# Kernel tuning notes

Hardware: AMD Instinct MI355X
Metric: run time of the kernel (lower is better)

The kernel has to match this reference:

```python
import jax, jax.numpy as jnp
import numpy as np

CANVAS = 512
SCORE_THR = 0.02
NMS_THR = 0.45
LVTOP = 1000      # cfg['lvtop'] for mm source
IMTOP = 200       # cfg['imtop']
NMS_PRE = 2000    # fixed pre-NMS candidate cap (static shape for jit)
NUM_CLASSES = 80
STRIDES = [8, 16, 32, 64, 128, 256, 512]
AR3 = [False, True, True, True, True, False, False]


def _make_priors():
    # get_scales(512): smallest=0.04, rmin=0.1, rmax=0.9, n=7
    smallest, rmin, rmax, n = 0.04, 0.1, 0.9, 7
    step = (rmax - rmin) / (n - 2)
    scales = [smallest] + [rmin + i * step for i in range(n)]
    sz = np.round(np.array(scales) * CANVAS).astype(np.int64)
    pr, lvlen = [], []
    for i, s in enumerate(STRIDES):
        fs = CANVAS // s
        ratios = [1.0, 2.0, 0.5] + ([3.0, 1.0 / 3.0] if AR3[i] else [])
        wh = [(sz[i] * np.sqrt(r), sz[i] / np.sqrt(r)) for r in ratios]
        extra = np.sqrt(float(sz[i]) * float(sz[i + 1]))  # sqrt(sz[i+1]/sz[i])*sz[i]
        wh.insert(1, (extra, extra))
        wh = np.array(wh, np.float32)            # [na, 2]
        xs = (np.arange(fs, dtype=np.float32) + 0.5) * s
        cx, cy = np.meshgrid(xs, xs)             # rows index y
        ctr = np.stack([cx, cy], -1)[:, :, None, :]  # [fs, fs, 1, 2]
        na = wh.shape[0]
        p = np.concatenate([np.broadcast_to(ctr, (fs, fs, na, 2)),
                            np.broadcast_to(wh, (fs, fs, na, 2))], -1).reshape(-1, 4)
        pr.append(p)
        lvlen.append(p.shape[0])
    return np.concatenate(pr).astype(np.float32), lvlen

PRIORS_NP, LVLEN = _make_priors()   # total 24564, lvlen=[16384,6144,1536,384,96,16,4]


def setup_inputs() -> dict:
    key = jax.random.key(0)
    k1, k2 = jax.random.split(key)
    A = PRIORS_NP.shape[0]
    cls_logits = jax.random.normal(k1, (4, A, NUM_CLASSES + 1), dtype=jnp.float32)
    reg = jax.random.normal(k2, (4, A, 4), dtype=jnp.float32)
    priors = jnp.asarray(PRIORS_NP)
    return {"cls_logits": cls_logits, "reg": reg, "priors": priors}


def _pairwise_iou(b):  # b: [K,4] xyxy
    area = (b[:, 2] - b[:, 0]) * (b[:, 3] - b[:, 1])
    lt = jnp.maximum(b[:, None, :2], b[None, :, :2])
    rb = jnp.minimum(b[:, None, 2:], b[None, :, 2:])
    wh = jnp.clip(rb - lt, 0.0)
    inter = wh[..., 0] * wh[..., 1]
    return inter / jnp.maximum(area[:, None] + area[None, :] - inter, 1e-6)


def _nms_keep(b):  # boxes sorted by descending score, class-offset applied
    m = _pairwise_iou(b) * jnp.triu(jnp.ones((NMS_PRE, NMS_PRE), b.dtype), 1)
    def body(sup, i):
        sup = sup | ((~sup[i]) & (m[i] > NMS_THR))
        return sup, None
    sup, _ = jax.lax.scan(body, jnp.zeros((NMS_PRE,), bool), jnp.arange(NMS_PRE))
    return ~sup


def reference(cls_logits, reg, priors):
    N = cls_logits.shape[0]
    C = NUM_CLASSES
    # softmax, background class is LAST (bckg_class_first=False for mm source)
    scr = jax.nn.softmax(cls_logits, axis=-1)[..., :-1]
    scr = jnp.where(scr > SCORE_THR, scr, 0.0)  # score threshold (fidx filter)
    # per-level top-k over flattened (anchor, class) pairs  [post.top_per_level]
    vals_l, anch_l, cls_l = [], [], []
    start = 0
    for lv in LVLEN:
        f = scr[:, start:start + lv, :].reshape(N, lv * C)
        k = min(LVTOP, lv * C)
        v, idx = jax.lax.top_k(f, k)
        vals_l.append(v)
        anch_l.append(start + idx // C)
        cls_l.append(idx % C)
        start += lv
    vals = jnp.concatenate(vals_l, 1)
    anch = jnp.concatenate(anch_l, 1)
    cls = jnp.concatenate(cls_l, 1)
    # fixed-size pre-NMS cap (static shapes under jit)
    v2, sel = jax.lax.top_k(vals, NMS_PRE)
    anch = jnp.take_along_axis(anch, sel, 1)
    cls = jnp.take_along_axis(cls, sel, 1)
    # decode boxes  [post.decode_boxes, mults=(0.1, 0.2), clamp=True]
    p = priors[anch]                                 # [N,K,4] cxcywh
    r = jnp.take_along_axis(reg, anch[..., None], 1)  # [N,K,4]
    cx = p[..., 0] + r[..., 0] * 0.1 * p[..., 2]
    cy = p[..., 1] + r[..., 1] * 0.1 * p[..., 3]
    w = p[..., 2] * jnp.exp(r[..., 2] * 0.2)
    h = p[..., 3] * jnp.exp(r[..., 3] * 0.2)
    boxes = jnp.stack([cx - w / 2, cy - h / 2, cx + w / 2, cy + h / 2], -1)
    boxes = jnp.clip(boxes, 0.0, float(CANVAS))
    # class-aware NMS via class offsets
    nb = boxes + cls.astype(boxes.dtype)[..., None] * (2.0 * CANVAS)
    keep = jax.vmap(_nms_keep)(nb)                   # [N,K] bool
    fs = jnp.where(keep & (v2 > 0), v2, 0.0)
    fv, fi = jax.lax.top_k(fs, IMTOP)                # imtop
    fb = jnp.take_along_axis(boxes, fi[..., None], 1)
    fc = jnp.take_along_axis(cls, fi, 1)
    fb = jnp.where(fv[..., None] > 0, fb, 0.0)
    return fb, fv, fc
```

## Files before the change

kernel.cpp:

```cpp
#include <hip/hip_runtime.h>
#include <hip/hip_bf16.h>
#include <math.h>

typedef unsigned long long u64;
typedef unsigned int u32;

#define A_TOTAL 24564
#define NCLS 80
#define NIMG 4
#define NPRE 2000
#define NLV 7
#define HBUCKETS 1024
#define BEXP_BASE 0x3CA3
#define TOTAL_G (NIMG * A_TOTAL)
#define FA 64
#define FT 256
#define NBLK_F ((TOTAL_G + FA - 1) / FA)
#define POOL_CAP_MAX 4096
#define CAPSEL 4608
#define MROWS 512
#define FTILES (MROWS / 16)

__device__ __constant__ int c_klv[NLV] = {1000,1000,1000,1000,1000,1000,320};

#define WS_HIST      0
#define WS_MCOUNT    114688
#define WS_BCOUNT    114800
#define WS_ZERO_END  114912
#define WS_PCOUNT    114912
#define WS_MAIN      121280
#define WS_BND       350656
#define WS_BOXES     1268160
#define WS_CLS       1396160
#define WS_SCORE     1428160
#define WS_MASK      1460160
#define WS_POOL      3508160

#define NZERO_W (WS_ZERO_END / 4)

__device__ inline u64 shfl_u64(u64 v, int src) {
  int lo = __shfl((int)(u32)(v & 0xFFFFFFFFULL), src);
  int hi = __shfl((int)(u32)(v >> 32), src);
  return ((u64)(u32)hi << 32) | (u32)lo;
}

__device__ inline int score_bucket(u32 bits) {
  int b = (int)(bits >> 16) - BEXP_BASE;
  return b < 0 ? 0 : (b > HBUCKETS - 1 ? HBUCKETS - 1 : b);
}

__device__ inline int level_of(int a) {
  return (a < 16384) ? 0 : (a < 22528) ? 1 : (a < 24064) ? 2 :
         (a < 24448) ? 3 : (a < 24544) ? 4 : (a < 24560) ? 5 : 6;
}

__global__ __launch_bounds__(256) void k_zero(u32* __restrict__ p) {
  int i = blockIdx.x * 256 + threadIdx.x;
  if (i < NZERO_W) p[i] = 0;
}

__device__ inline void score20(const float* __restrict__ logits, int g, int q,
                               float (&e)[20], float& rt) {
  const float* row = logits + (size_t)g * 81;
  float x[20];
#pragma unroll
  for (int i = 0; i < 20; ++i) x[i] = row[q + 4 * i];
  float x80 = (q == 3) ? row[80] : 0.f;
  float mloc = x[0];
#pragma unroll
  for (int i = 1; i < 20; ++i) mloc = fmaxf(mloc, x[i]);
  if (q == 3) mloc = fmaxf(mloc, x80);
  float m = fmaxf(mloc, __shfl_xor(mloc, 1));
  m = fmaxf(m, __shfl_xor(m, 2));
  float tq = 0.f;
#pragma unroll
  for (int i = 0; i < 20; ++i) { e[i] = expf(x[i] - m); tq += e[i]; }
  if (q == 3) tq += expf(x80 - m);
  float t = tq + __shfl_xor(tq, 1);
  t = t + __shfl_xor(t, 2);
  rt = 1.0f / t;
}

__device__ inline void wave_find_cut(const u32* __restrict__ h, int k, int lane,
                                     int& cx, int& cy) {
  u32 s = 0;
#pragma unroll
  for (int i = 0; i < 16; ++i) s += h[lane * 16 + i];
  u32 S = s;
#pragma unroll
  for (int o = 1; o < 64; o <<= 1) {
    u32 t = (u32)__shfl_down((int)S, o);
    if (lane + o < 64) S += t;
  }
  u32 total = (u32)__shfl((int)S, 0);
  if (total <= (u32)k) { cx = -1; cy = 0; return; }
  u64 bm = __ballot(S >= (u32)k);
  int L0 = 63 - (int)__clzll((long long)bm);
  u32 Sup = (u32)__shfl_down((int)S, 1);
  if (lane == 63) Sup = 0;
  int rcx = 0, rcy = 0;
  if (lane == L0) {
    u32 cum = Sup;
    for (int i = 15; i >= 0; --i) {
      u32 c = h[lane * 16 + i];
      if (cum + c >= (u32)k) { rcx = lane * 16 + i; rcy = k - (int)cum; break; }
      cum += c;
    }
  }
  cx = __shfl(rcx, L0);
  cy = __shfl(rcy, L0);
}

__global__ __launch_bounds__(FT) void k_fused(const float* __restrict__ logits,
                                              u32* __restrict__ histG,
                                              u64* __restrict__ pool,
                                              u32* __restrict__ pcount, int cap) {
  __shared__ u64 sh8_[HBUCKETS / 2];
  u32* sh = (u32*)sh8_;
  __shared__ int nm;
  int tid = threadIdx.x, bx = blockIdx.x;
  for (int b = tid; b < HBUCKETS; b += FT) sh[b] = 0;
  if (tid == 0) nm = 0;
  int la = tid >> 2, q = tid & 3;
  int g = bx * FA + la;
  bool valid = g < TOTAL_G;
  int g0 = bx * FA;
  int seg0 = (g0 / A_TOTAL) * NLV + level_of(g0 % A_TOTAL);
  int seg = seg0, a = 0;
  float e[20];
  float rt = 0.f;
  if (valid) {
    int img = g / A_TOTAL;
    a = g - img * A_TOTAL;
    seg = img * NLV + level_of(a);
    score20(logits, g, q, e, rt);
  }
  int uniform = __syncthreads_and((int)(!valid || seg == seg0));
  if (valid) {
    u32* hdst = uniform ? sh : (histG + (size_t)seg * HBUCKETS);
    u32 wmask = 0;
#pragma unroll
    for (int i = 0; i < 20; ++i) {
      float s = e[i] * rt;
      if (s > 0.02f) wmask |= (1u << i);
    }
    int cnt = __popc(wmask);
    int basep = 0;
    if (cnt) basep = atomicAdd(&nm, cnt);
    while (wmask) {
      int i = __ffs(wmask) - 1;
      wmask &= wmask - 1;
      float s = e[i] * rt;
      u32 bits = __float_as_uint(s);
      atomicAdd(&hdst[score_bucket(bits)], 1u);
      if (basep < cap)
        pool[(size_t)bx * cap + basep] =
            ((u64)bits << 32) | (u64)(0xFFFFFFFFu - (u32)(a * NCLS + q + 4 * i));
      ++basep;
    }
  }
  __syncthreads();
  if (uniform) {
    u64* hseg8 = (u64*)(histG + (size_t)seg0 * HBUCKETS);
    for (int b = tid; b < HBUCKETS / 2; b += FT) {
      u64 v = sh8_[b];
      if (v) atomicAdd(&hseg8[b], v);
    }
  }
  if (tid == 0) pcount[bx] = (u32)nm;
}

__global__ __launch_bounds__(FT) void k_filter(const float* __restrict__ logits,
                                               const u64* __restrict__ pool,
                                               const u32* __restrict__ pcount,
                                               const u32* __restrict__ histG, int cap,
                                               u64* __restrict__ mainG, u32* __restrict__ mcount,
                                               u64* __restrict__ bndG, u32* __restrict__ bcount) {
  __shared__ int lcx4[4];
  __shared__ u64 mk[1024]; __shared__ unsigned char msg_[1024];
  __shared__ u64 bkl[256]; __shared__ unsigned char bsg[256];
  __shared__ int nm, nb, cm[4], cb[4], basem[4], baseb[4], wm[4], wb[4];
  int tid = threadIdx.x, bx = blockIdx.x;
  if (tid < 4) { cm[tid] = 0; cb[tid] = 0; wm[tid] = 0; wb[tid] = 0; }
  if (tid == 0) { nm = 0; nb = 0; }
  int g0 = bx * FA;
  int img0 = g0 / A_TOTAL;
  int alo = g0 - img0 * A_TOTAL;
  int gN = g0 + FA - 1; if (gN > TOTAL_G - 1) gN = TOTAL_G - 1;
  int seg_lo = img0 * NLV + level_of(alo);
  int seg_hi = (gN / A_TOTAL) * NLV + level_of(gN % A_TOTAL);
  int nseg = seg_hi - seg_lo + 1;
  int wid = tid >> 6, lane = tid & 63;
  if (wid < nseg) {
    int cx, cy;
    wave_find_cut(histG + (size_t)(seg_lo + wid) * HBUCKETS,
                  c_klv[(seg_lo + wid) % NLV], lane, cx, cy);
    if (lane == 0) lcx4[wid] = cx;
  }
  __syncthreads();
  int n = (int)pcount[bx];
  if (n <= cap) {
    for (int t = tid; t < n; t += FT) {
      u64 key = pool[(size_t)bx * cap + t];
      u32 bits = (u32)(key >> 32);
      u32 flat = 0xFFFFFFFFu - (u32)(key & 0xFFFFFFFFULL);
      int a = (int)(flat / NCLS);
      int img = (a >= alo) ? img0 : img0 + 1;
      int seg = img * NLV + level_of(a);
      int si = seg - seg_lo;
      int ctx = lcx4[si];
      int bk = score_bucket(bits);
      if (ctx < 0 || bk > ctx) {
        int p = atomicAdd(&nm, 1);
        if (p < 1024) { mk[p] = key; msg_[p] = (unsigned char)si; atomicAdd(&cm[si], 1); }
        else { u32 pg = atomicAdd(&mcount[seg], 1u); if (pg < 1024) mainG[(size_t)seg * 1024 + pg] = key; }
      } else if (bk == ctx) {
        int p = atomicAdd(&nb, 1);
        if (p < 256) { bkl[p] = key; bsg[p] = (unsigned char)si; atomicAdd(&cb[si], 1); }
        else { u32 pg = atomicAdd(&bcount[seg], 1u); if (pg < 4096) bndG[(size_t)seg * 4096 + pg] = key; }
      }
    }
  } else {
    int la = tid >> 2, q = tid & 3;
    int g = g0 + la;
    if (g < TOTAL_G) {
      int img = g / A_TOTAL;
      int a = g - img * A_TOTAL;
      int seg = img * NLV + level_of(a);
      int si = seg - seg_lo;
      int ctx = lcx4[si];
      float e[20];
      float rt;
      score20(logits, g, q, e, rt);
      for (int i = 0; i < 20; ++i) {
        float s = e[i] * rt;
        if (s > 0.02f) {
          u32 bits = __float_as_uint(s);
          int bk = score_bucket(bits);
          u64 key = ((u64)bits << 32) | (u64)(0xFFFFFFFFu - (u32)(a * NCLS + q + 4 * i));
          if (ctx < 0 || bk > ctx) {
            int p = atomicAdd(&nm, 1);
            if (p < 1024) { mk[p] = key; msg_[p] = (unsigned char)si; atomicAdd(&cm[si], 1); }
            else { u32 pg = atomicAdd(&mcount[seg], 1u); if (pg < 1024) mainG[(size_t)seg * 1024 + pg] = key; }
          } else if (bk == ctx) {
            int p = atomicAdd(&nb, 1);
            if (p < 256) { bkl[p] = key; bsg[p] = (unsigned char)si; atomicAdd(&cb[si], 1); }
            else { u32 pg = atomicAdd(&bcount[seg], 1u); if (pg < 4096) bndG[(size_t)seg * 4096 + pg] = key; }
          }
        }
      }
    }
  }
  __syncthreads();
  if (tid < nseg) {
    if (cm[tid] > 0) basem[tid] = (int)atomicAdd(&mcount[seg_lo + tid], (u32)cm[tid]);
    if (cb[tid] > 0) baseb[tid] = (int)atomicAdd(&bcount[seg_lo + tid], (u32)cb[tid]);
  }
  __syncthreads();
  int tm = nm < 1024 ? nm : 1024;
  for (int idx = tid; idx < tm; idx += FT) {
    int si = msg_[idx];
    int slot = atomicAdd(&wm[si], 1);
    int d = basem[si] + slot;
    if (d < 1024) mainG[(size_t)(seg_lo + si) * 1024 + d] = mk[idx];
  }
  int tb = nb < 256 ? nb : 256;
  for (int idx = tid; idx < tb; idx += FT) {
    int si = bsg[idx];
    int slot = atomicAdd(&wb[si], 1);
    int d = baseb[si] + slot;
    if (d < 4096) bndG[(size_t)(seg_lo + si) * 4096 + d] = bkl[idx];
  }
}

__global__ __launch_bounds__(1024) void k_gsel(const u32* __restrict__ histG,
                                               const u64* __restrict__ mainG,
                                               const u32* __restrict__ mcount,
                                               const u64* __restrict__ bndG,
                                               const u32* __restrict__ bcount,
                                               const float4* __restrict__ priors,
                                               const float4* __restrict__ reg,
                                               float4* __restrict__ boxesG,
                                               int* __restrict__ clsG,
                                               float* __restrict__ scoreG) {
  int img = blockIdx.x;
  int tid = threadIdx.x, wid = tid >> 6, lane = tid & 63;
  __shared__ u32 H[HBUCKETS];
  __shared__ u32 cntb[HBUCKETS];
  __shared__ u32 Sarr[HBUCKETS];
  __shared__ u32 cnt2[HBUCKETS];
  __shared__ u64 sel[CAPSEL];
  __shared__ int lcx[NLV], lcy[NLV];
  __shared__ int sh_gx, sh_gy, sh_cC, sh_cand, sh_sgx;
  if (tid == 0) { sh_cC = 0; sh_cand = 0; sh_sgx = -1; }
  if (wid < NLV) {
    int cx, cy;
    wave_find_cut(histG + (size_t)(img * NLV + wid) * HBUCKETS, c_klv[wid], lane, cx, cy);
    if (lane == 0) { lcx[wid] = cx; lcy[wid] = cy; }
  }
  __syncthreads();
  for (int b = tid; b < HBUCKETS; b += 1024) {
    u32 acc = 0;
#pragma unroll
    for (int l = 0; l < NLV; ++l) {
      u32 h = histG[(size_t)(img * NLV + l) * HBUCKETS + b];
      int cx = lcx[l];
      if (cx < 0 || b > cx) acc += h;
      else if (b == cx) acc += (u32)lcy[l];
    }
    H[b] = acc;
    cntb[b] = 0;
    cnt2[b] = 0;
  }
  __syncthreads();
  if (wid == 0) {
    int gx, gy;
    wave_find_cut(H, NPRE, lane, gx, gy);
    if (lane == 0) { sh_gx = gx; sh_gy = gy; }
  }
  __syncthreads();
  int gx = sh_gx, gy = sh_gy;
  int mcap[NLV], bcap[NLV];
#pragma unroll
  for (int l = 0; l < NLV; ++l) {
    int c = (int)mcount[img * NLV + l]; mcap[l] = c > 1024 ? 1024 : c;
    int bc = (lcx[l] >= 0) ? (int)bcount[img * NLV + l] : 0; bcap[l] = bc > 4096 ? 4096 : bc;
  }
  for (int l = 0; l < NLV; ++l)
    for (int t = tid; t < mcap[l]; t += 1024) {
      u64 key = mainG[(size_t)(img * NLV + l) * 1024 + t];
      int b = score_bucket((u32)(key >> 32));
      if (gx < 0 || b > gx) atomicAdd(&cntb[b], 1u);
      else if (b == gx) atomicAdd(&sh_cC, 1);
    }
  for (int l = 0; l < NLV; ++l) {
    const u64* B = bndG + (size_t)(img * NLV + l) * 4096;
    for (int t = tid; t < bcap[l]; t += 1024) {
      u64 key = B[t];
      int r = 0;
      for (int u = 0; u < bcap[l]; ++u) r += (B[u] > key) ? 1 : 0;
      if (r < lcy[l]) {
        int b = lcx[l];
        if (gx < 0 || b > gx) atomicAdd(&cntb[b], 1u);
        else if (b == gx) atomicAdd(&sh_cC, 1);
      }
    }
  }
  __syncthreads();
  for (int b = tid; b < HBUCKETS; b += 1024) Sarr[b] = cntb[b];
  __syncthreads();
  {
    u32* A = Sarr; u32* B = H;
    for (int o = 1; o < HBUCKETS; o <<= 1) {
      for (int b = tid; b < HBUCKETS; b += 1024)
        B[b] = A[b] + ((b + o < HBUCKETS) ? A[b + o] : 0u);
      __syncthreads();
      u32* tmp = A; A = B; B = tmp;
    }
  }
  int cA = (int)Sarr[0];
  int cC = sh_cC;
  int cand = (gx >= 0) ? cC : 0;
  int sgx = -1;
  if (gx >= 0 && cA + cC > CAPSEL) {
    for (int b = tid; b < HBUCKETS; b += 1024) H[b] = 0;
    __syncthreads();
    for (int l = 0; l < NLV; ++l)
      for (int t = tid; t < mcap[l]; t += 1024) {
        u64 key = mainG[(size_t)(img * NLV + l) * 1024 + t];
        u32 bits = (u32)(key >> 32);
        if (score_bucket(bits) == gx) atomicAdd(&H[(bits >> 6) & 1023], 1u);
      }
    for (int l = 0; l < NLV; ++l) {
      if (lcx[l] != gx) continue;
      const u64* B = bndG + (size_t)(img * NLV + l) * 4096;
      for (int t = tid; t < bcap[l]; t += 1024) {
        u64 key = B[t];
        int r = 0;
        for (int u = 0; u < bcap[l]; ++u) r += (B[u] > key) ? 1 : 0;
        if (r < lcy[l]) atomicAdd(&H[((u32)(key >> 32) >> 6) & 1023], 1u);
      }
    }
    __syncthreads();
    if (wid == 0) {
      int a1, a2;
      wave_find_cut(H, gy, lane, a1, a2);
      if (lane == 0) sh_sgx = a1;
    }
    __syncthreads();
    sgx = sh_sgx;
    if (sgx >= 0) {
      for (int s2 = tid; s2 < HBUCKETS; s2 += 1024)
        if (s2 >= sgx) { u32 v = H[s2]; if (v) atomicAdd(&sh_cand, (int)v); }
      __syncthreads();
      cand = sh_cand;
    }
    if (cA + cand > CAPSEL) cand = CAPSEL - cA;
  }
  __syncthreads();
  for (int l = 0; l < NLV; ++l)
    for (int t = tid; t < mcap[l]; t += 1024) {
      u64 key = mainG[(size_t)(img * NLV + l) * 1024 + t];
      u32 bits = (u32)(key >> 32);
      int b = score_bucket(bits);
      bool inc = false; int segbase = 0, seglen = 0;
      if (gx < 0 || b > gx) {
        inc = true; segbase = (int)(Sarr[b] - cntb[b]); seglen = (int)cntb[b];
      } else if (b == gx) {
        inc = (sgx < 0) || ((int)((bits >> 6) & 1023) >= sgx);
        segbase = (int)Sarr[b]; seglen = cand;
      }
      if (inc) {
        int slot = (int)atomicAdd(&cnt2[b], 1u);
        if (slot < seglen) sel[segbase + slot] = key;
      }
    }
  for (int l = 0; l < NLV; ++l) {
    const u64* B = bndG + (size_t)(img * NLV + l) * 4096;
    for (int t = tid; t < bcap[l]; t += 1024) {
      u64 key = B[t];
      int r = 0;
      for (int u = 0; u < bcap[l]; ++u) r += (B[u] > key) ? 1 : 0;
      if (r >= lcy[l]) continue;
      u32 bits = (u32)(key >> 32);
      int b = lcx[l];
      bool inc = false; int segbase = 0, seglen = 0;
      if (gx < 0 || b > gx) {
        inc = true; segbase = (int)(Sarr[b] - cntb[b]); seglen = (int)cntb[b];
      } else if (b == gx) {
        inc = (sgx < 0) || ((int)((bits >> 6) & 1023) >= sgx);
        segbase = (int)Sarr[b]; seglen = cand;
      }
      if (inc) {
        int slot = (int)atomicAdd(&cnt2[b], 1u);
        if (slot < seglen) sel[segbase + slot] = key;
      }
    }
  }
  __syncthreads();
  int total = cA + cand;
// ... 170 lines not shown
            remv |= fbm[r][wl];
            if (lane == 0 && cnt < 216) keptList[cnt] = (u32)i;
            ++cnt;
          }
        }
        if (lane == 0 && (cnt >= 200 || ft == 124)) {
          sh_stop = 1;
          sh_cnt = cnt < 216 ? cnt : 216;
          if (cnt < 200) sh_done = 1;
        }
        if (ft == 124 && lane < 32) sh_remv[lane] = remv;
      }
      __syncthreads();
      if (sh_stop) break;
    }
  }
  __syncthreads();
  int nK = sh_cnt;
  if (sh_done && nK < 200) {
    int base = tid * 8;
    bool sb[8];
    int scnt = 0;
#pragma unroll
    for (int e = 0; e < 8; ++e) {
      int i = base + e;
      bool sup = (i < NPRE) && ((sh_remv[i >> 6] >> (i & 63)) & 1ULL);
      sb[e] = sup;
      scnt += sup ? 1 : 0;
    }
    kpref[tid + 1] = scnt;
    if (tid == 0) kpref[0] = 0;
    __syncthreads();
    if (tid == 0) {
      int acc = 0;
      for (int t = 1; t <= 256; ++t) { acc += kpref[t]; kpref[t] = acc; }
    }
    __syncthreads();
    int sp = kpref[tid];
#pragma unroll
    for (int e = 0; e < 8; ++e) {
      int i = base + e;
      if (i < NPRE && sb[e]) S[sp++] = (unsigned short)i;
    }
    __syncthreads();
    if (tid < 200) {
      float fv = 0.f;
      float4 fb = make_float4(0.f, 0.f, 0.f, 0.f);
      int fc;
      if (tid < nK) {
        int idx = (int)keptList[tid];
        fv = scoreG[(size_t)img * NPRE + idx];
        fb = boxesG[(size_t)img * NPRE + idx];
        fc = clsG[(size_t)img * NPRE + idx];
      } else {
        int idx = S[tid - nK];
        fc = clsG[(size_t)img * NPRE + idx];
      }
      float* fbo = out + (size_t)img * 800 + tid * 4;
      fbo[0] = fb.x; fbo[1] = fb.y; fbo[2] = fb.z; fbo[3] = fb.w;
      out[3200 + (size_t)img * 200 + tid] = fv;
      out[4000 + (size_t)img * 200 + tid] = (float)fc;
    }
  } else {
    if (tid < 200) {
      int idx = (int)keptList[tid];
      float fv = scoreG[(size_t)img * NPRE + idx];
      float4 fb = boxesG[(size_t)img * NPRE + idx];
      int fc = clsG[(size_t)img * NPRE + idx];
      float* fbo = out + (size_t)img * 800 + tid * 4;
      fbo[0] = fb.x; fbo[1] = fb.y; fbo[2] = fb.z; fbo[3] = fb.w;
      out[3200 + (size_t)img * 200 + tid] = fv;
      out[4000 + (size_t)img * 200 + tid] = (float)fc;
    }
  }
}

extern "C" void kernel_launch(void* const* d_in, const int* in_sizes, int n_in,
                              void* d_out, int out_size, void* d_ws, size_t ws_size,
                              hipStream_t stream) {
  const float* logits = (const float*)d_in[0];
  const float4* reg = (const float4*)d_in[1];
  const float4* priors = (const float4*)d_in[2];
  char* ws = (char*)d_ws;
  u32* hist = (u32*)(ws + WS_HIST);
  u32* mcount = (u32*)(ws + WS_MCOUNT);
  u32* bcount = (u32*)(ws + WS_BCOUNT);
  u32* pcount = (u32*)(ws + WS_PCOUNT);
  u64* mainL = (u64*)(ws + WS_MAIN);
  u64* bndL = (u64*)(ws + WS_BND);
  float4* boxes = (float4*)(ws + WS_BOXES);
  int* cls = (int*)(ws + WS_CLS);
  float* score = (float*)(ws + WS_SCORE);
  u64* mask = (u64*)(ws + WS_MASK);
  u64* pool = (u64*)(ws + WS_POOL);

  size_t avail = ws_size > (size_t)WS_POOL ? ws_size - (size_t)WS_POOL : 0;
  int cap = (int)(avail / ((size_t)NBLK_F * 8));
  if (cap > POOL_CAP_MAX) cap = POOL_CAP_MAX;

  k_zero<<<(NZERO_W + 255) / 256, 256, 0, stream>>>((u32*)d_ws);
  k_fused<<<NBLK_F, FT, 0, stream>>>(logits, hist, pool, pcount, cap);
  k_filter<<<NBLK_F, FT, 0, stream>>>(logits, pool, pcount, hist, cap,
                                      mainL, mcount, bndL, bcount);
  k_gsel<<<NIMG, 1024, 0, stream>>>(hist, mainL, mcount, bndL, bcount,
                                    priors, reg, boxes, cls, score);
  k_mask<<<NIMG * (MROWS / 4), 256, 0, stream>>>(boxes, cls, mask);
  k_scanfinal<<<NIMG, 256, 0, stream>>>(mask, boxes, cls, score, (float*)d_out);
}
```

Before: 109.7 us.

## Fuse all pipeline stages into one persistent cooperative kernel with grid syncs

Replaces the six separate launches (zero, score/histogram, filter, global select, NMS mask, scan/final) with one persistent cooperative kernel. It loops over work groups per stage and separates the stages with grid.sync. The aim is to remove per-launch overhead and inter-kernel gaps. In exchange, the select stage now runs on 256-thread blocks instead of 1024, so its quadratic ranking loops get fewer threads per image, and each grid-wide barrier has its own cost. The old multi-kernel path stays as a fallback if the cooperative launch fails.

Result: slower. 438.1 us (+299.6%).

```diff
diff --git a/kernel.cpp b/kernel.cpp
--- a/kernel.cpp
+++ b/kernel.cpp
@@ -1,6 +1,9 @@
 #include <hip/hip_runtime.h>
 #include <hip/hip_bf16.h>
+#include <hip/hip_cooperative_groups.h>
 #include <math.h>
+
+namespace cg = cooperative_groups;
 
 typedef unsigned long long u64;
 typedef unsigned int u32;
@@ -14,8 +17,9 @@
 #define BEXP_BASE 0x3CA3
 #define TOTAL_G (NIMG * A_TOTAL)
 #define FA 64
-#define FT 256
-#define NBLK_F ((TOTAL_G + FA - 1) / FA)
+#define TPB 256
+#define NGRP ((TOTAL_G + FA - 1) / FA)
+#define GRID_MAX 1024
 #define POOL_CAP_MAX 4096
 #define CAPSEL 4608
 #define MROWS 512
@@ -52,11 +56,6 @@
 __device__ inline int level_of(int a) {
   return (a < 16384) ? 0 : (a < 22528) ? 1 : (a < 24064) ? 2 :
          (a < 24448) ? 3 : (a < 24544) ? 4 : (a < 24560) ? 5 : 6;
-}
-
-__global__ __launch_bounds__(256) void k_zero(u32* __restrict__ p) {
-  int i = blockIdx.x * 256 + threadIdx.x;
-  if (i < NZERO_W) p[i] = 0;
 }
 
 __device__ inline void score20(const float* __restrict__ logits, int g, int q,
@@ -111,15 +110,598 @@
   cy = __shfl(rcy, L0);
 }
 
-__global__ __launch_bounds__(FT) void k_fused(const float* __restrict__ logits,
-                                              u32* __restrict__ histG,
-                                              u64* __restrict__ pool,
-                                              u32* __restrict__ pcount, int cap) {
+#define SMEM_BYTES 16384
+
+__global__ __launch_bounds__(TPB, 4) void k_all(const float* __restrict__ logits,
+                                                const float4* __restrict__ reg,
+                                                const float4* __restrict__ priors,
+                                                char* __restrict__ ws, int cap,
+                                                float* __restrict__ out) {
+  cg::grid_group grid = cg::this_grid();
+  __shared__ __align__(16) char SMEM[SMEM_BYTES];
+  __shared__ int si[40];
+  __shared__ int lcx7[NLV], lcy7[NLV];
+
+  u32* histG = (u32*)(ws + WS_HIST);
+  u32* mcount = (u32*)(ws + WS_MCOUNT);
+  u32* bcount = (u32*)(ws + WS_BCOUNT);
+  u32* pcount = (u32*)(ws + WS_PCOUNT);
+  u64* mainG = (u64*)(ws + WS_MAIN);
+  u64* bndG = (u64*)(ws + WS_BND);
+  float4* boxesG = (float4*)(ws + WS_BOXES);
+  int* clsG = (int*)(ws + WS_CLS);
+  float* scoreG = (float*)(ws + WS_SCORE);
+  u64* maskG = (u64*)(ws + WS_MASK);
+  u64* pool = (u64*)(ws + WS_POOL);
+
+  int bx = blockIdx.x, tid = threadIdx.x;
+  int wid = tid >> 6, lane = tid & 63;
+  int GB = gridDim.x;
+
+  for (int i = bx * TPB + tid; i < NZERO_W; i += GB * TPB) ((u32*)ws)[i] = 0;
+  grid.sync();
+
+  {
+    u64* sh8 = (u64*)SMEM;
+    u32* sh = (u32*)SMEM;
+    for (int grp = bx; grp < NGRP; grp += GB) {
+      for (int b = tid; b < HBUCKETS; b += TPB) sh[b] = 0;
+      if (tid == 0) si[0] = 0;
+      int la = tid >> 2, q = tid & 3;
+      int g = grp * FA + la;
+      bool valid = g < TOTAL_G;
+      int g0 = grp * FA;
+      int seg0 = (g0 / A_TOTAL) * NLV + level_of(g0 % A_TOTAL);
+      int seg = seg0, a = 0;
+      float e[20];
+      float rt = 0.f;
+      if (valid) {
+        int img = g / A_TOTAL;
+        a = g - img * A_TOTAL;
+        seg = img * NLV + level_of(a);
+        score20(logits, g, q, e, rt);
+      }
+      int uniform = __syncthreads_and((int)(!valid || seg == seg0));
+      if (valid) {
+        u32* hdst = uniform ? sh : (histG + (size_t)seg * HBUCKETS);
+        u32 wmask = 0;
+#pragma unroll
+        for (int i = 0; i < 20; ++i) {
+          float s = e[i] * rt;
+          if (s > 0.02f) wmask |= (1u << i);
+        }
+        int cnt = __popc(wmask);
+        int basep = 0;
+        if (cnt) basep = atomicAdd(&si[0], cnt);
+        while (wmask) {
+          int i = __ffs(wmask) - 1;
+          wmask &= wmask - 1;
+          float s = e[i] * rt;
+          u32 bits = __float_as_uint(s);
+          atomicAdd(&hdst[score_bucket(bits)], 1u);
+          if (basep < cap)
+            pool[(size_t)grp * cap + basep] =
+                ((u64)bits << 32) | (u64)(0xFFFFFFFFu - (u32)(a * NCLS + q + 4 * i));
+          ++basep;
+        }
+      }
+      __syncthreads();
+      if (uniform) {
+        u64* hseg8 = (u64*)(histG + (size_t)seg0 * HBUCKETS);
+        for (int b = tid; b < HBUCKETS / 2; b += TPB) {
+          u64 v = sh8[b];
+          if (v) atomicAdd(&hseg8[b], v);
+        }
+      }
+      if (tid == 0) pcount[grp] = (u32)si[0];
+      __syncthreads();
+    }
+  }
+  grid.sync();
+
+  {
+    u64* mk = (u64*)SMEM;
+    u64* bkl = (u64*)(SMEM + 8192);
+    unsigned char* msg_ = (unsigned char*)(SMEM + 10240);
+    unsigned char* bsg = (unsigned char*)(SMEM + 11264);
+    int* nm = &si[0]; int* nb = &si[1];
+    int* cm = &si[2]; int* cb = &si[6];
+    int* basem = &si[10]; int* baseb = &si[14];
+    int* wm = &si[18]; int* wb = &si[22];
+    int* lcx4 = &si[26];
+    for (int grp = bx; grp < NGRP; grp += GB) {
+      if (tid < 4) { cm[tid] = 0; cb[tid] = 0; wm[tid] = 0; wb[tid] = 0; }
+      if (tid == 0) { *nm = 0; *nb = 0; }
+      int g0 = grp * FA;
+      int img0 = g0 / A_TOTAL;
+      int alo = g0 - img0 * A_TOTAL;
+      int gN = g0 + FA - 1; if (gN > TOTAL_G - 1) gN = TOTAL_G - 1;
+      int seg_lo = img0 * NLV + level_of(alo);
+      int seg_hi = (gN / A_TOTAL) * NLV + level_of(gN % A_TOTAL);
+      int nseg = seg_hi - seg_lo + 1;
+      if (wid < nseg) {
+        int cx, cy;
+        wave_find_cut(histG + (size_t)(seg_lo + wid) * HBUCKETS,
+                      c_klv[(seg_lo + wid) % NLV], lane, cx, cy);
+        if (lane == 0) lcx4[wid] = cx;
+      }
+      __syncthreads();
+      int n = (int)pcount[grp];
+      if (n <= cap) {
+        for (int t = tid; t < n; t += TPB) {
+          u64 key = pool[(size_t)grp * cap + t];
+          u32 bits = (u32)(key >> 32);
+          u32 flat = 0xFFFFFFFFu - (u32)(key & 0xFFFFFFFFULL);
+          int a = (int)(flat / NCLS);
+          int img = (a >= alo) ? img0 : img0 + 1;
+          int seg = img * NLV + level_of(a);
+          int sl = seg - seg_lo;
+          int ctx = lcx4[sl];
+          int bk = score_bucket(bits);
+          if (ctx < 0 || bk > ctx) {
+            int p = atomicAdd(nm, 1);
+            if (p < 1024) { mk[p] = key; msg_[p] = (unsigned char)sl; atomicAdd(&cm[sl], 1); }
+            else { u32 pg = atomicAdd(&mcount[seg], 1u); if (pg < 1024) mainG[(size_t)seg * 1024 + pg] = key; }
+          } else if (bk == ctx) {
+            int p = atomicAdd(nb, 1);
+            if (p < 256) { bkl[p] = key; bsg[p] = (unsigned char)sl; atomicAdd(&cb[sl], 1); }
+            else { u32 pg = atomicAdd(&bcount[seg], 1u); if (pg < 4096) bndG[(size_t)seg * 4096 + pg] = key; }
+          }
+        }
+      } else {
+        int la = tid >> 2, q = tid & 3;
+        int g = g0 + la;
+        if (g < TOTAL_G) {
+          int img = g / A_TOTAL;
+          int a = g - img * A_TOTAL;
+          int seg = img * NLV + level_of(a);
+          int sl = seg - seg_lo;
+          int ctx = lcx4[sl];
+          float e[20];
+          float rt;
+          score20(logits, g, q, e, rt);
+          for (int i = 0; i < 20; ++i) {
+            float s = e[i] * rt;
+            if (s > 0.02f) {
+              u32 bits = __float_as_uint(s);
+              int bk = score_bucket(bits);
+              u64 key = ((u64)bits << 32) | (u64)(0xFFFFFFFFu - (u32)(a * NCLS + q + 4 * i));
+              if (ctx < 0 || bk > ctx) {
+                int p = atomicAdd(nm, 1);
+                if (p < 1024) { mk[p] = key; msg_[p] = (unsigned char)sl; atomicAdd(&cm[sl], 1); }
+                else { u32 pg = atomicAdd(&mcount[seg], 1u); if (pg < 1024) mainG[(size_t)seg * 1024 + pg] = key; }
+              } else if (bk == ctx) {
+                int p = atomicAdd(nb, 1);
+                if (p < 256) { bkl[p] = key; bsg[p] = (unsigned char)sl; atomicAdd(&cb[sl], 1); }
+                else { u32 pg = atomicAdd(&bcount[seg], 1u); if (pg < 4096) bndG[(size_t)seg * 4096 + pg] = key; }
+              }
+            }
+          }
+        }
+      }
+      __syncthreads();
+      if (tid < nseg) {
+        if (cm[tid] > 0) basem[tid] = (int)atomicAdd(&mcount[seg_lo + tid], (u32)cm[tid]);
+        if (cb[tid] > 0) baseb[tid] = (int)atomicAdd(&bcount[seg_lo + tid], (u32)cb[tid]);
+      }
+      __syncthreads();
+      int tm = *nm < 1024 ? *nm : 1024;
+      for (int idx = tid; idx < tm; idx += TPB) {
+        int sl = msg_[idx];
+        int slot = atomicAdd(&wm[sl], 1);
+        int d = basem[sl] + slot;
+        if (d < 1024) mainG[(size_t)(seg_lo + sl) * 1024 + d] = mk[idx];
+      }
+      int tb = *nb < 256 ? *nb : 256;
+      for (int idx = tid; idx < tb; idx += TPB) {
+        int sl = bsg[idx];
+        int slot = atomicAdd(&wb[sl], 1);
+        int d = baseb[sl] + slot;
+        if (d < 4096) bndG[(size_t)(seg_lo + sl) * 4096 + d] = bkl[idx];
+      }
+      __syncthreads();
+    }
+  }
+  grid.sync();
+
+  for (int img = bx; img < NIMG; img += GB) {
+    u32* H = (u32*)SMEM;
+    u32* cntb = (u32*)(SMEM + 4096);
+    u32* Sarr = (u32*)(SMEM + 8192);
+    u32* cnt2 = (u32*)(SMEM + 12288);
+    u64* selI = pool + (size_t)img * CAPSEL;
+    u64* sel2I = pool + (size_t)(NIMG + img) * CAPSEL;
+    int* sh_gx = &si[0]; int* sh_gy = &si[1]; int* sh_cC = &si[2];
+    int* sh_cand = &si[3]; int* sh_sgx = &si[4];
+    __syncthreads();
+    if (tid == 0) { *sh_cC = 0; *sh_cand = 0; *sh_sgx = -1; }
+    for (int l = wid; l < NLV; l += 4) {
+      int cx, cy;
+      wave_find_cut(histG + (size_t)(img * NLV + l) * HBUCKETS, c_klv[l], lane, cx, cy);
+      if (lane == 0) { lcx7[l] = cx; lcy7[l] = cy; }
+    }
+    __syncthreads();
+    for (int b = tid; b < HBUCKETS; b += TPB) {
+      u32 acc = 0;
+#pragma unroll
+      for (int l = 0; l < NLV; ++l) {
+        u32 h = histG[(size_t)(img * NLV + l) * HBUCKETS + b];
+        int cx = lcx7[l];
+        if (cx < 0 || b > cx) acc += h;
+        else if (b == cx) acc += (u32)lcy7[l];
+      }
+      H[b] = acc;
+      cntb[b] = 0;
+      cnt2[b] = 0;
+    }
+    __syncthreads();
+    if (wid == 0) {
+      int gx, gy;
+      wave_find_cut(H, NPRE, lane, gx, gy);
+      if (lane == 0) { *sh_gx = gx; *sh_gy = gy; }
+    }
+    __syncthreads();
+    int gx = *sh_gx, gy = *sh_gy;
+    int mcap[NLV], bcap[NLV];
+#pragma unroll
+    for (int l = 0; l < NLV; ++l) {
+      int c = (int)mcount[img * NLV + l]; mcap[l] = c > 1024 ? 1024 : c;
+      int bc = (lcx7[l] >= 0) ? (int)bcount[img * NLV + l] : 0; bcap[l] = bc > 4096 ? 4096 : bc;
+    }
+    for (int l = 0; l < NLV; ++l)
+      for (int t = tid; t < mcap[l]; t += TPB) {
+        u64 key = mainG[(size_t)(img * NLV + l) * 1024 + t];
+        int b = score_bucket((u32)(key >> 32));
+        if (gx < 0 || b > gx) atomicAdd(&cntb[b], 1u);
+        else if (b == gx) atomicAdd(sh_cC, 1);
+      }
+    for (int l = 0; l < NLV; ++l) {
+      const u64* B = bndG + (size_t)(img * NLV + l) * 4096;
+      for (int t = tid; t < bcap[l]; t += TPB) {
+        u64 key = B[t];
+        int r = 0;
+        for (int u = 0; u < bcap[l]; ++u) r += (B[u] > key) ? 1 : 0;
+        if (r < lcy7[l]) {
+          int b = lcx7[l];
+          if (gx < 0 || b > gx) atomicAdd(&cntb[b], 1u);
+          else if (b == gx) atomicAdd(sh_cC, 1);
+        }
+      }
+    }
+    __syncthreads();
+    for (int b = tid; b < HBUCKETS; b += TPB) Sarr[b] = cntb[b];
+    __syncthreads();
+    {
+      u32* A = Sarr; u32* B2 = H;
+      for (int o = 1; o < HBUCKETS; o <<= 1) {
+        for (int b = tid; b < HBUCKETS; b += TPB)
+          B2[b] = A[b] + ((b + o < HBUCKETS) ? A[b + o] : 0u);
+        __syncthreads();
+        u32* tmp = A; A = B2; B2 = tmp;
+      }
+    }
+    int cA = (int)Sarr[0];
+    int cC = *sh_cC;
+    int cand = (gx >= 0) ? cC : 0;
+    int sgx = -1;
+    if (gx >= 0 && cA + cC > CAPSEL) {
+      for (int b = tid; b < HBUCKETS; b += TPB) H[b] = 0;
+      __syncthreads();
+      for (int l = 0; l < NLV; ++l)
+        for (int t = tid; t < mcap[l]; t += TPB) {
+          u64 key = mainG[(size_t)(img * NLV + l) * 1024 + t];
+          u32 bits = (u32)(key >> 32);
+          if (score_bucket(bits) == gx) atomicAdd(&H[(bits >> 6) & 1023], 1u);
+        }
+      for (int l = 0; l < NLV; ++l) {
+        if (lcx7[l] != gx) continue;
+        const u64* B = bndG + (size_t)(img * NLV + l) * 4096;
+        for (int t = tid; t < bcap[l]; t += TPB) {
+          u64 key = B[t];
+          int r = 0;
+          for (int u = 0; u < bcap[l]; ++u) r += (B[u] > key) ? 1 : 0;
+          if (r < lcy7[l]) atomicAdd(&H[((u32)(key >> 32) >> 6) & 1023], 1u);
+        }
+      }
+      __syncthreads();
+      if (wid == 0) {
+        int a1, a2;
+        wave_find_cut(H, gy, lane, a1, a2);
+        if (lane == 0) *sh_sgx = a1;
+      }
+      __syncthreads();
+      sgx = *sh_sgx;
+      if (sgx >= 0) {
+        for (int s2 = tid; s2 < HBUCKETS; s2 += TPB)
+          if (s2 >= sgx) { u32 v = H[s2]; if (v) atomicAdd(sh_cand, (int)v); }
+        __syncthreads();
+        cand = *sh_cand;
+      }
+      if (cA + cand > CAPSEL) cand = CAPSEL - cA;
+    }
+    __syncthreads();
+    for (int l = 0; l < NLV; ++l)
+      for (int t = tid; t < mcap[l]; t += TPB) {
+        u64 key = mainG[(size_t)(img * NLV + l) * 1024 + t];
+        u32 bits = (u32)(key >> 32);
+        int b = score_bucket(bits);
+        bool inc = false; int segbase = 0, seglen = 0;
+        if (gx < 0 || b > gx) {
+          inc = true; segbase = (int)(Sarr[b] - cntb[b]); seglen = (int)cntb[b];
+        } else if (b == gx) {
+          inc = (sgx < 0) || ((int)((bits >> 6) & 1023) >= sgx);
+          segbase = (int)Sarr[b]; seglen = cand;
+        }
+        if (inc) {
+          int slot = (int)atomicAdd(&cnt2[b], 1u);
+          if (slot < seglen) selI[segbase + slot] = key;
+        }
+      }
+    for (int l = 0; l < NLV; ++l) {
+      const u64* B = bndG + (size_t)(img * NLV + l) * 4096;
+      for (int t = tid; t < bcap[l]; t += TPB) {
+        u64 key = B[t];
+        int r = 0;
+        for (int u = 0; u < bcap[l]; ++u) r += (B[u] > key) ? 1 : 0;
+        if (r >= lcy7[l]) continue;
+        u32 bits = (u32)(key >> 32);
+        int b = lcx7[l];
+        bool inc = false; int segbase = 0, seglen = 0;
+        if (gx < 0 || b > gx) {
+          inc = true; segbase = (int)(Sarr[b] - cntb[b]); seglen = (int)cntb[b];
+        } else if (b == gx) {
+          inc = (sgx < 0) || ((int)((bits >> 6) & 1023) >= sgx);
+          segbase = (int)Sarr[b]; seglen = cand;
+        }
+        if (inc) {
+          int slot = (int)atomicAdd(&cnt2[b], 1u);
+          if (slot < seglen) selI[segbase + slot] = key;
+        }
+      }
+    }
+    __syncthreads();
+    int total = cA + cand;
+    if (total > CAPSEL) total = CAPSEL;
+    for (int t = tid; t < total; t += TPB) {
+      u64 key = selI[t];
+      u32 bits = (u32)(key >> 32);
+      int b = score_bucket(bits);
+      int segbase, seglen;
+      if (gx >= 0 && b == gx) { segbase = (int)Sarr[b]; seglen = cand; }
+      else { segbase = (int)(Sarr[b] - cntb[b]); seglen = (int)cntb[b]; }
+      int r = 0;
+      for (int u = 0; u < seglen; ++u) r += (selI[segbase + u] > key) ? 1 : 0;
+      sel2I[segbase + r] = key;
+    }
+    __syncthreads();
+    for (int t = tid; t < NPRE; t += TPB) {
+      u64 key = (t < total) ? sel2I[t] : 0ULL;
+      float4 bx4 = make_float4(0.f, 0.f, 0.f, 0.f);
+      int c = -1;
+      float sc = 0.f;
+      if (key != 0ULL) {
+        sc = __uint_as_float((u32)(key >> 32));
+        u32 flat = 0xFFFFFFFFu - (u32)(key & 0xFFFFFFFFULL);
+        int a = (int)(flat / NCLS);
+        c = (int)(flat % NCLS);
+        float4 p = priors[a];
+        float4 r = reg[(size_t)img * A_TOTAL + a];
+        float cx = p.x + (r.x * 0.1f) * p.z;
+        float cy = p.y + (r.y * 0.1f) * p.w;
+        float w = p.z * expf(r.z * 0.2f);
+        float h = p.w * expf(r.w * 0.2f);
+        bx4.x = fminf(fmaxf(cx - w * 0.5f, 0.f), 512.f);
+        bx4.y = fminf(fmaxf(cy - h * 0.5f, 0.f), 512.f);
+        bx4.z = fminf(fmaxf(cx + w * 0.5f, 0.f), 512.f);
+        bx4.w = fminf(fmaxf(cy + h * 0.5f, 0.f), 512.f);
+      }
+      boxesG[(size_t)img * NPRE + t] = bx4;
+      clsG[(size_t)img * NPRE + t] = c;
+      scoreG[(size_t)img * NPRE + t] = sc;
+    }
+    __syncthreads();
+  }
+  grid.sync();
+
+  for (int wk = bx; wk < NIMG * (MROWS / 4); wk += GB) {
+    int img = wk / (MROWS / 4);
+    int rb = (wk % (MROWS / 4)) * 4;
+    const float4* BB = boxesG + (size_t)img * NPRE;
+    const int* CC = clsG + (size_t)img * NPRE;
+    int i = rb + wid;
+    float4 bi = BB[i];
+    int ci = CC[i];
+    float ai = (bi.z - bi.x) * (bi.w - bi.y);
+    u64* mrow = maskG + ((size_t)img * MROWS + i) * 32;
+    for (int ch = 0; ch < 32; ++ch) {
+      int j = ch * 64 + lane;
+      bool pred = false;
+      if (j < NPRE && j > i && CC[j] == ci) {
+        float4 bj = BB[j];
+        float xx1 = fmaxf(bi.x, bj.x), yy1 = fmaxf(bi.y, bj.y);
+        float xx2 = fminf(bi.z, bj.z), yy2 = fminf(bi.w, bj.w);
+        float ww = fmaxf(xx2 - xx1, 0.f), hh = fmaxf(yy2 - yy1, 0.f);
+        float inter = ww * hh;
+        float aj = (bj.z - bj.x) * (bj.w - bj.y);
+        float iou = inter / fmaxf(ai + aj - inter, 1e-6f);
+        pred = iou > 0.45f;
+      }
+      u64 word = __ballot(pred);
+      if (lane == 0) mrow[ch] = word;
+    }
+  }
+  grid.sync();
+
+  for (int img = bx; img < NIMG; img += GB) {
+    u64* fbm = (u64*)SMEM;
+    u32* keptList = (u32*)(SMEM + 4096);
+    unsigned short* S = (unsigned short*)(SMEM + 4960);
+    int* kpref = (int*)(SMEM + 8960);
+    u64* sh_remv = (u64*)(SMEM + 10240);
+    int* sh_cnt = &si[0]; int* sh_done = &si[1];
+    int* sh_fall = &si[2]; int* sh_stop = &si[3];
+    __syncthreads();
+    if (tid == 0) { *sh_cnt = 0; *sh_done = 0; *sh_fall = 0; *sh_stop = 0; }
+    __syncthreads();
+    u64 remv = 0;
+    int cnt = 0;
+    if (tid < 64) {
+      int wl = lane & 31;
+      const u64* M = maskG + (size_t)img * MROWS * 32;
+      u64 cur[16], nxt[16], bc[16];
+      u64 curword = 0;
+#pragma unroll
+      for (int r = 0; r < 16; ++r) cur[r] = M[(size_t)r * 32 + wl];
+      for (int t = 0; t < FTILES; ++t) {
+        int spanw = t >> 2;
+        if ((t & 3) == 0) curword = shfl_u64(remv, spanw);
+        if (t < FTILES - 1) {
+#pragma unroll
+          for (int r = 0; r < 16; ++r) nxt[r] = M[(size_t)((t + 1) * 16 + r) * 32 + wl];
+        }
+#pragma unroll
+        for (int r = 0; r < 16; ++r) bc[r] = shfl_u64(cur[r], spanw);
+#pragma unroll
+        for (int r = 0; r < 16; ++r) {
+          int i = t * 16 + r;
+          if (!((curword >> (i & 63)) & 1ULL)) {
+            remv |= cur[r];
+            curword |= bc[r];
+            if (lane == 0 && cnt < 216) keptList[cnt] = (u32)i;
+            ++cnt;
+          }
+        }
+#pragma unroll
+        for (int r = 0; r < 16; ++r) cur[r] = nxt[r];
+        if (cnt >= 200) break;
+      }
+      if (lane == 0) { *sh_cnt = cnt < 216 ? cnt : 216; *sh_fall = (cnt < 200) ? 1 : 0; }
+    }
+    __syncthreads();
+    if (*sh_fall) {
+      for (int ft = FTILES; ft < 125; ++ft) {
+        for (int r = wid; r < 16; r += 4) {
+          int i = ft * 16 + r;
+          float4 bi = boxesG[(size_t)img * NPRE + i];
+          int ci = clsG[(size_t)img * NPRE + i];
+          float ai = (bi.z - bi.x) * (bi.w - bi.y);
+          for (int ch = 0; ch < 32; ++ch) {
+            int j = ch * 64 + lane;
+            bool pred = false;
+            if (j < NPRE && j > i && clsG[(size_t)img * NPRE + j] == ci) {
+              float4 bj = boxesG[(size_t)img * NPRE + j];
+              float xx1 = fmaxf(bi.x, bj.x), yy1 = fmaxf(bi.y, bj.y);
+              float xx2 = fminf(bi.z, bj.z), yy2 = fminf(bi.w, bj.w);
+              float ww = fmaxf(xx2 - xx1, 0.f), hh = fmaxf(yy2 - yy1, 0.f);
+              float inter = ww * hh;
+              float aj = (bj.z - bj.x) * (bj.w - bj.y);
+              float iou = inter / fmaxf(ai + aj - inter, 1e-6f);
+              pred = iou > 0.45f;
+            }
+            u64 word = __ballot(pred);
+            if (lane == 0) fbm[r * 32 + ch] = word;
+          }
+        }
+        __syncthreads();
+        if (tid < 64) {
+          int wl = lane & 31;
+#pragma unroll
+          for (int r = 0; r < 16; ++r) {
+            int i = ft * 16 + r;
+            u64 rm = shfl_u64(remv, i >> 6);
+            if (!((rm >> (i & 63)) & 1ULL)) {
+              remv |= fbm[r * 32 + wl];
+              if (lane == 0 && cnt < 216) keptList[cnt] = (u32)i;
+              ++cnt;
+            }
+          }
+          if (lane == 0 && (cnt >= 200 || ft == 124)) {
+            *sh_stop = 1;
+            *sh_cnt = cnt < 216 ? cnt : 216;
+            if (cnt < 200) *sh_done = 1;
+          }
+          if (ft == 124 && lane < 32) sh_remv[lane] = remv;
+        }
+        __syncthreads();
+        if (*sh_stop) break;
+      }
+    }
+    __syncthreads();
+    int nK = *sh_cnt;
+    if (*sh_done && nK < 200) {
+      int base = tid * 8;
+      bool sb[8];
+      int scnt = 0;
+#pragma unroll
+      for (int e2 = 0; e2 < 8; ++e2) {
+        int i = base + e2;
+        bool sup = (i < NPRE) && ((sh_remv[i >> 6] >> (i & 63)) & 1ULL);
+        sb[e2] = sup;
+        scnt += sup ? 1 : 0;
+      }
+      kpref[tid + 1] = scnt;
+      if (tid == 0) kpref[0] = 0;
+      __syncthreads();
+      if (tid == 0) {
+        int acc = 0;
+        for (int t = 1; t <= TPB; ++t) { acc += kpref[t]; kpref[t] = acc; }
+      }
+      __syncthreads();
+      int sp = kpref[tid];
+#pragma unroll
+      for (int e2 = 0; e2 < 8; ++e2) {
+        int i = base + e2;
+        if (i < NPRE && sb[e2]) S[sp++] = (unsigned short)i;
+      }
+      __syncthreads();
+      if (tid < 200) {
+        float fv = 0.f;
+        float4 fb = make_float4(0.f, 0.f, 0.f, 0.f);
+        int fc;
+        if (tid < nK) {
+          int idx = (int)keptList[tid];
+          fv = scoreG[(size_t)img * NPRE + idx];
+          fb = boxesG[(size_t)img * NPRE + idx];
+          fc = clsG[(size_t)img * NPRE + idx];
+        } else {
+          int idx = S[tid - nK];
+          fc = clsG[(size_t)img * NPRE + idx];
+        }
+        float* fbo = out + (size_t)img * 800 + tid * 4;
+        fbo[0] = fb.x; fbo[1] = fb.y; fbo[2] = fb.z; fbo[3] = fb.w;
+        out[3200 + (size_t)img * 200 + tid] = fv;
+        out[4000 + (size_t)img * 200 + tid] = (float)fc;
+      }
+    } else {
+      if (tid < 200) {
+        int idx = (int)keptList[tid];
+        float fv = scoreG[(size_t)img * NPRE + idx];
+        float4 fb = boxesG[(size_t)img * NPRE + idx];
+        int fc = clsG[(size_t)img * NPRE + idx];
+        float* fbo = out + (size_t)img * 800 + tid * 4;
+        fbo[0] = fb.x; fbo[1] = fb.y; fbo[2] = fb.z; fbo[3] = fb.w;
+        out[3200 + (size_t)img * 200 + tid] = fv;
+        out[4000 + (size_t)img * 200 + tid] = (float)fc;
+      }
+    }
+    __syncthreads();
+  }
+}
+
+__global__ __launch_bounds__(256) void k_zero(u32* __restrict__ p) {
+  int i = blockIdx.x * 256 + threadIdx.x;
+  if (i < NZERO_W) p[i] = 0;
+}
+
+__global__ __launch_bounds__(256) void k_fused(const float* __restrict__ logits,
+                                               u32* __restrict__ histG,
+                                               u64* __restrict__ pool,
+                                               u32* __restrict__ pcount, int cap) {
   __shared__ u64 sh8_[HBUCKETS / 2];
   u32* sh = (u32*)sh8_;
   __shared__ int nm;
   int tid = threadIdx.x, bx = blockIdx.x;
-  for (int b = tid; b < HBUCKETS; b += FT) sh[b] = 0;
+  for (int b = tid; b < HBUCKETS; b += 256) sh[b] = 0;
   if (tid == 0) nm = 0;
   int la = tid >> 2, q = tid & 3;
   int g = bx * FA + la;
@@ -162,7 +744,7 @@
   __syncthreads();
   if (uniform) {
     u64* hseg8 = (u64*)(histG + (size_t)seg0 * HBUCKETS);
-    for (int b = tid; b < HBUCKETS / 2; b += FT) {
+    for (int b = tid; b < HBUCKETS / 2; b += 256) {
       u64 v = sh8_[b];
       if (v) atomicAdd(&hseg8[b], v);
     }
@@ -170,12 +752,12 @@
   if (tid == 0) pcount[bx] = (u32)nm;
 }
 
-__global__ __launch_bounds__(FT) void k_filter(const float* __restrict__ logits,
-                                               const u64* __restrict__ pool,
-                                               const u32* __restrict__ pcount,
-                                               const u32* __restrict__ histG, int cap,
-                                               u64* __restrict__ mainG, u32* __restrict__ mcount,
-                                               u64* __restrict__ bndG, u32* __restrict__ bcount) {
+__global__ __launch_bounds__(256) void k_filter(const float* __restrict__ logits,
+                                                const u64* __restrict__ pool,
+                                                const u32* __restrict__ pcount,
+                                                const u32* __restrict__ histG, int cap,
+                                                u64* __restrict__ mainG, u32* __restrict__ mcount,
+                                                u64* __restrict__ bndG, u32* __restrict__ bcount) {
   __shared__ int lcx4[4];
   __shared__ u64 mk[1024]; __shared__ unsigned char msg_[1024];
   __shared__ u64 bkl[256]; __shared__ unsigned char bsg[256];
@@ -200,23 +782,23 @@
   __syncthreads();
   int n = (int)pcount[bx];
   if (n <= cap) {
-    for (int t = tid; t < n; t += FT) {
+    for (int t = tid; t < n; t += 256) {
       u64 key = pool[(size_t)bx * cap + t];
       u32 bits = (u32)(key >> 32);
       u32 flat = 0xFFFFFFFFu - (u32)(key & 0xFFFFFFFFULL);
       int a = (int)(flat / NCLS);
       int img = (a >= alo) ? img0 : img0 + 1;
       int seg = img * NLV + level_of(a);
-      int si = seg - seg_lo;
-      int ctx = lcx4[si];
+      int si2 = seg - seg_lo;
+      int ctx = lcx4[si2];
       int bk = score_bucket(bits);
       if (ctx < 0 || bk > ctx) {
         int p = atomicAdd(&nm, 1);
-        if (p < 1024) { mk[p] = key; msg_[p] = (unsigned char)si; atomicAdd(&cm[si], 1); }
+        if (p < 1024) { mk[p] = key; msg_[p] = (unsigned char)si2; atomicAdd(&cm[si2], 1); }
         else { u32 pg = atomicAdd(&mcount[seg], 1u); if (pg < 1024) mainG[(size_t)seg * 1024 + pg] = key; }
       } else if (bk == ctx) {
         int p = atomicAdd(&nb, 1);
-        if (p < 256) { bkl[p] = key; bsg[p] = (unsigned char)si; atomicAdd(&cb[si], 1); }
+        if (p < 256) { bkl[p] = key; bsg[p] = (unsigned char)si2; atomicAdd(&cb[si2], 1); }
         else { u32 pg = atomicAdd(&bcount[seg], 1u); if (pg < 4096) bndG[(size_t)seg * 4096 + pg] = key; }
       }
     }
@@ -227,8 +809,8 @@
       int img = g / A_TOTAL;
       int a = g - img * A_TOTAL;
       int seg = img * NLV + level_of(a);
-      int si = seg - seg_lo;
-      int ctx = lcx4[si];
+      int si2 = seg - seg_lo;
+      int ctx = lcx4[si2];
       float e[20];
       float rt;
       score20(logits, g, q, e, rt);
@@ -240,11 +822,11 @@
           u64 key = ((u64)bits << 32) | (u64)(0xFFFFFFFFu - (u32)(a * NCLS + q + 4 * i));
           if (ctx < 0 || bk > ctx) {
             int p = atomicAdd(&nm, 1);
-            if (p < 1024) { mk[p] = key; msg_[p] = (unsigned char)si; atomicAdd(&cm[si], 1); }
+            if (p < 1024) { mk[p] = key; msg_[p] = (unsigned char)si2; atomicAdd(&cm[si2], 1); }
             else { u32 pg = atomicAdd(&mcount[seg], 1u); if (pg < 1024) mainG[(size_t)seg * 1024 + pg] = key; }
           } else if (bk == ctx) {
             int p = atomicAdd(&nb, 1);
-            if (p < 256) { bkl[p] = key; bsg[p] = (unsigned char)si; atomicAdd(&cb[si], 1); }
+            if (p < 256) { bkl[p] = key; bsg[p] = (unsigned char)si2; atomicAdd(&cb[si2], 1); }
             else { u32 pg = atomicAdd(&bcount[seg], 1u); if (pg < 4096) bndG[(size_t)seg * 4096 + pg] = key; }
           }
         }
@@ -258,18 +840,18 @@
   }
   __syncthreads();
   int tm = nm < 1024 ? nm : 1024;
-  for (int idx = tid; idx < tm; idx += FT) {
-    int si = msg_[idx];
-    int slot = atomicAdd(&wm[si], 1);
-    int d = basem[si] + slot;
-    if (d < 1024) mainG[(size_t)(seg_lo + si) * 1024 + d] = mk[idx];
+  for (int idx = tid; idx < tm; idx += 256) {
+    int si2 = msg_[idx];
+    int slot = atomicAdd(&wm[si2], 1);
+    int d = basem[si2] + slot;
+    if (d < 1024) mainG[(size_t)(seg_lo + si2) * 1024 + d] = mk[idx];
   }
   int tb = nb < 256 ? nb : 256;
-  for (int idx = tid; idx < tb; idx += FT) {
-    int si = bsg[idx];
-    int slot = atomicAdd(&wb[si], 1);
-    int d = baseb[si] + slot;
-    if (d < 4096) bndG[(size_t)(seg_lo + si) * 4096 + d] = bkl[idx];
+  for (int idx = tid; idx < tb; idx += 256) {
+    int si2 = bsg[idx];
+    int slot = atomicAdd(&wb[si2], 1);
+    int d = baseb[si2] + slot;
+    if (d < 4096) bndG[(size_t)(seg_lo + si2) * 4096 + d] = bkl[idx];
   }
 }
 
@@ -350,12 +932,12 @@
   for (int b = tid; b < HBUCKETS; b += 1024) Sarr[b] = cntb[b];
   __syncthreads();
   {
-    u32* A = Sarr; u32* B = H;
+    u32* A = Sarr; u32* B2 = H;
     for (int o = 1; o < HBUCKETS; o <<= 1) {
       for (int b = tid; b < HBUCKETS; b += 1024)
-        B[b] = A[b] + ((b + o < HBUCKETS) ? A[b + o] : 0u);
-      __syncthreads();
-      u32* tmp = A; A = B; B = tmp;
+        B2[b] = A[b] + ((b + o < HBUCKETS) ? A[b + o] : 0u);
+      __syncthreads();
+      u32* tmp = A; A = B2; B2 = tmp;
     }
   }
   int cA = (int)Sarr[0];
@@ -692,6 +1274,30 @@
   const float4* reg = (const float4*)d_in[1];
   const float4* priors = (const float4*)d_in[2];
   char* ws = (char*)d_ws;
+  float* outp = (float*)d_out;
+
+  size_t avail = ws_size > (size_t)WS_POOL ? ws_size - (size_t)WS_POOL : 0;
+  int cap = (int)(avail / ((size_t)NGRP * 8));
+  if (cap > POOL_CAP_MAX) cap = POOL_CAP_MAX;
+
+  int dev = 0;
+  hipGetDevice(&dev);
+  int nCU = 0;
+  hipDeviceGetAttribute(&nCU, hipDeviceAttributeMultiprocessorCount, dev);
+  int maxB = 0;
+  hipError_t oe = hipOccupancyMaxActiveBlocksPerMultiprocessor(
+      &maxB, (const void*)k_all, TPB, 0);
+  int grid = (oe == hipSuccess && maxB > 0 && nCU > 0) ? maxB * nCU : 0;
+  if (grid > GRID_MAX) grid = GRID_MAX;
+
+  if (grid >= 16) {
+    void* args[] = {(void*)&logits, (void*)&reg, (void*)&priors,
+                    (void*)&ws, (void*)&cap, (void*)&outp};
+    hipError_t le = hipLaunchCooperativeKernel((void*)k_all, dim3(grid), dim3(TPB),
+                                               args, 0, stream);
+    if (le == hipSuccess) return;
+  }
+
   u32* hist = (u32*)(ws + WS_HIST);
   u32* mcount = (u32*)(ws + WS_MCOUNT);
   u32* bcount = (u32*)(ws + WS_BCOUNT);
@@ -704,14 +1310,10 @@
   u64* mask = (u64*)(ws + WS_MASK);
   u64* pool = (u64*)(ws + WS_POOL);
 
-  size_t avail = ws_size > (size_t)WS_POOL ? ws_size - (size_t)WS_POOL : 0;
-  int cap = (int)(avail / ((size_t)NBLK_F * 8));
-  if (cap > POOL_CAP_MAX) cap = POOL_CAP_MAX;
-
   k_zero<<<(NZERO_W + 255) / 256, 256, 0, stream>>>((u32*)d_ws);
-  k_fused<<<NBLK_F, FT, 0, stream>>>(logits, hist, pool, pcount, cap);
-  k_filter<<<NBLK_F, FT, 0, stream>>>(logits, pool, pcount, hist, cap,
-                                      mainL, mcount, bndL, bcount);
+  k_fused<<<NGRP, 256, 0, stream>>>(logits, hist, pool, pcount, cap);
+  k_filter<<<NGRP, 256, 0, stream>>>(logits, pool, pcount, hist, cap,
+                                     mainL, mcount, bndL, bcount);
   k_gsel<<<NIMG, 1024, 0, stream>>>(hist, mainL, mcount, bndL, bcount,
                                     priors, reg, boxes, cls, score);
   k_mask<<<NIMG * (MROWS / 4), 256, 0, stream>>>(boxes, cls, mask);
```
